# Kernel optimization log

Hardware: AMD Instinct MI355X
Metric: run time of the kernel (lower is better)

Reference implementation:

```python
import jax, jax.numpy as jnp
import numpy as np

# dims
B, L, H, NH, D = 512, 200, 128, 4, 32      # batch, seq_len, hidden, heads (gnn & fcb), head dim H/NH
FT, TP, IP = 32, 64, 200                    # first_taxonomy_num, taxonomy/item nodes per graph
NHOP, NB = 2, 2                             # n_hop gnn layers, gip_block_nums
SH, FH = 512, 256                           # scb_hidden_units, fcb_hidden_units
ITEMS, TAX = 100001, 2000                   # item vocab (+pad row 0), taxonomy vocab
NT, NI = B * TP, B * IP                     # total taxonomy / item nodes in batched forest
DEG_I, DEG_T = 4, 2                         # in-degree per taxonomy node for i2t / t2t edges


def _ln(x, g, b, eps=1e-8):
    m = jnp.mean(x, -1, keepdims=True)
    v = jnp.mean((x - m) ** 2, -1, keepdims=True)
    return (x - m) / jnp.sqrt(v + eps) * g + b


def _gat(src_h, dst_h, es, ed, W, al, ar, bias):
    """DGL GATConv (eval mode): shared fc, leaky_relu(0.2) scores, segment softmax,
    identity residual (in == heads*out), bias, ReLU activation."""
    fs = (src_h @ W).reshape(-1, NH, D)                 # [Ns,NH,D]
    fd = (dst_h @ W).reshape(-1, NH, D)                 # [Nd,NH,D]
    el = jnp.sum(fs * al, -1)                           # [Ns,NH]
    er = jnp.sum(fd * ar, -1)                           # [Nd,NH]
    e = jax.nn.leaky_relu(el[es] + er[ed], 0.2)         # [E,NH]
    emax = jax.ops.segment_max(e, ed, num_segments=NT)
    a = jnp.exp(e - emax[ed])
    s = jax.ops.segment_sum(a, ed, num_segments=NT)
    alpha = a / s[ed]                                   # [E,NH]
    rst = jax.ops.segment_sum(alpha[..., None] * fs[es], ed, num_segments=NT)
    rst = rst + dst_h.reshape(-1, NH, D) + bias.reshape(NH, D)
    return jax.nn.relu(rst).reshape(-1, NH * D)


def _forward(item_embed, tax_embed, scb_ln_g, scb_ln_b, scb_w1, scb_w2, fcb_ln_g, fcb_ln_b,
             fcb_w1, fcb_w2, fcb_w3, wv, gi_w, gi_al, gi_ar, gi_b, gt_w, gt_al, gt_ar, gt_b,
             liw_g, liw_b, int_g, int_b, uni_w,
             seq, root, i2t_src, i2t_dst, t2t_src, t2t_dst, item_ids, tax_ids):
    # --- global intention: mixer-style blocks over the item sequence ---
    V = item_embed[seq]                                           # [B,L,H]
    for i in range(NB):
        nv = _ln(V, scb_ln_g[i], scb_ln_b[i])
        t = jax.nn.gelu(jnp.einsum('blh,ls->bhs', nv, scb_w1[i]), approximate=False)
        vs = nv + jnp.einsum('bhs,sl->blh', t, scb_w2[i])         # seq-mixing block
        nvs = _ln(vs, fcb_ln_g[i], fcb_ln_b[i])
        xh = nvs.reshape(B, L, NH, D)                             # fcb heads share w1/w2
        y = jax.nn.gelu(jnp.einsum('blkc,cf->blkf', xh, fcb_w1[i]), approximate=False)
        y = jnp.einsum('blkf,fc->blkc', y, fcb_w2[i]).reshape(B, L, H)
        V = nvs + y @ fcb_w3[i]
    alpha = jax.nn.softmax(V @ wv, axis=1)                        # [B,L]
    g = jnp.sum(alpha[..., None] * V, axis=1)                     # [B,H]
    # --- local intention: multi-hop hetero GAT on batched item-taxonomy forest ---
    item_h = item_embed[item_ids]                                 # [NI,H]
    tax_h = tax_embed[tax_ids]                                    # [NT,H]
    acc = jnp.zeros_like(tax_h)
    for hop in range(NHOP):
        t_i = _gat(item_h, tax_h, i2t_src, i2t_dst, gi_w[hop], gi_al[hop], gi_ar[hop], gi_b[hop])
        t_t = _gat(tax_h, tax_h, t2t_src, t2t_dst, gt_w[hop], gt_al[hop], gt_ar[hop], gt_b[hop])
        tax_h = t_i + t_t                                         # HeteroGraphConv 'sum'
        acc = acc + tax_h                                         # k_list accumulation
    total = acc / NHOP                                            # average over hops
    offs = jnp.arange(B) * TP                                     # batched-graph offsets (graph_taxonomy)
    valid = root != -1
    local = jnp.where(valid[..., None], total[jnp.clip(root, 0) + offs[:, None]], 0.0)  # [B,FT,H]
    # --- fuse global + local ---
    mul = jnp.einsum('bfh,bh->bf', local, g)                      # [B,FT]
    w = jax.nn.softmax(jnp.where(mul != 0, _ln(mul, liw_g, liw_b), -jnp.inf), axis=-1)
    intention = _ln(g + jnp.sum(w[..., None] * local, axis=1), int_g, int_b)
    return (intention @ uni_w) @ item_embed.T                     # [B, ITEMS]


def setup_inputs():
    key = jax.random.key(0)
    ks = jax.random.split(key, 32)
    nrm = lambda i, sh: jax.random.normal(ks[i], sh, jnp.float32) * 0.05
    inp = {}
    inp['seq'] = jax.random.randint(ks[0], (B, L), 0, ITEMS)
    inp['root'] = jax.random.randint(ks[1], (B, FT), 0, TP)       # all valid roots
    i2t_dst = jnp.repeat(jnp.arange(NT), DEG_I)
    inp['i2t_dst'] = i2t_dst
    inp['i2t_src'] = (i2t_dst // TP) * IP + jax.random.randint(ks[2], (NT * DEG_I,), 0, IP)
    t2t_dst = jnp.repeat(jnp.arange(NT), DEG_T)
    inp['t2t_dst'] = t2t_dst
    inp['t2t_src'] = (t2t_dst // TP) * TP + jax.random.randint(ks[3], (NT * DEG_T,), 0, TP)
    inp['item_ids'] = jax.random.randint(ks[4], (NI,), 1, ITEMS)
    inp['tax_ids'] = jax.random.randint(ks[5], (NT,), 1, TAX)
    inp['item_embed'] = nrm(6, (ITEMS, H)).at[0].set(0.0)         # padding_idx=0
    inp['tax_embed'] = nrm(7, (TAX, H)).at[0].set(0.0)
    inp['scb_ln_g'] = jnp.ones((NB, H)); inp['scb_ln_b'] = jnp.zeros((NB, H))
    inp['scb_w1'] = nrm(8, (NB, L, SH)); inp['scb_w2'] = nrm(9, (NB, SH, L))
    inp['fcb_ln_g'] = jnp.ones((NB, H)); inp['fcb_ln_b'] = jnp.zeros((NB, H))
    inp['fcb_w1'] = nrm(10, (NB, D, FH)); inp['fcb_w2'] = nrm(11, (NB, FH, D))
    inp['fcb_w3'] = nrm(12, (NB, H, H))
    inp['wv'] = nrm(13, (H,))
    inp['gi_w'] = nrm(14, (NHOP, H, H)); inp['gi_al'] = nrm(15, (NHOP, NH, D))
    inp['gi_ar'] = nrm(16, (NHOP, NH, D)); inp['gi_b'] = nrm(17, (NHOP, H))
    inp['gt_w'] = nrm(18, (NHOP, H, H)); inp['gt_al'] = nrm(19, (NHOP, NH, D))
    inp['gt_ar'] = nrm(20, (NHOP, NH, D)); inp['gt_b'] = nrm(21, (NHOP, H))
    inp['liw_g'] = jnp.ones((FT,)); inp['liw_b'] = jnp.zeros((FT,))
    inp['int_g'] = jnp.ones((H,)); inp['int_b'] = jnp.zeros((H,))
    inp['uni_w'] = nrm(22, (H, H))
    return inp


def reference(item_embed, tax_embed, scb_ln_g, scb_ln_b, scb_w1, scb_w2, fcb_ln_g, fcb_ln_b,
              fcb_w1, fcb_w2, fcb_w3, wv, gi_w, gi_al, gi_ar, gi_b, gt_w, gt_al, gt_ar, gt_b,
              liw_g, liw_b, int_g, int_b, uni_w,
              seq, root, i2t_src, i2t_dst, t2t_src, t2t_dst, item_ids, tax_ids):
    return _forward(item_embed, tax_embed, scb_ln_g, scb_ln_b, scb_w1, scb_w2, fcb_ln_g, fcb_ln_b,
                    fcb_w1, fcb_w2, fcb_w3, wv, gi_w, gi_al, gi_ar, gi_b, gt_w, gt_al, gt_ar, gt_b,
                    liw_g, liw_b, int_g, int_b, uni_w,
                    seq, root, i2t_src, i2t_dst, t2t_src, t2t_dst, item_ids, tax_ids)
```

## Files before the change

### kernel.cpp

```cpp
#include <hip/hip_runtime.h>
#include <hip/hip_bf16.h>

constexpr int TB = 512, TL = 200, TH = 128, TNH = 4, TD = 32;
constexpr int TFT = 32, TTP = 64, TIP = 200;
constexpr int TSH = 512, TFH = 256;
constexpr int TITEMS = 100001;
constexpr int TNT = TB * TTP;
constexpr int TNI = TB * TIP;
constexpr int TLP = 224;
constexpr int TIPAD = 100096;

typedef __attribute__((ext_vector_type(8))) short short8v;
typedef __attribute__((ext_vector_type(4))) float f32x4;

__device__ inline float gelu_fast(float x) {
    float u = x + 0.044715f * x * x * x;
    float e = exp2f(-2.302208f * u);
    return x / (1.0f + e);
}
__device__ inline unsigned short to_bf16u(float x) {
    __hip_bfloat16 h = __float2bfloat16(x);
    return *reinterpret_cast<unsigned short*>(&h);
}
__device__ inline float bfu_to_f(unsigned short u) {
    unsigned int x = ((unsigned int)u) << 16;
    return __uint_as_float(x);
}

__device__ inline float block_reduce_sum(float v, float* red) {
    for (int o = 32; o > 0; o >>= 1) v += __shfl_down(v, o, 64);
    int nw = blockDim.x >> 6;
    if ((threadIdx.x & 63) == 0) red[threadIdx.x >> 6] = v;
    __syncthreads();
    float r = 0.f;
    for (int w = 0; w < nw; ++w) r += red[w];
    __syncthreads();
    return r;
}

__global__ __launch_bounds__(256) void k_gather_bf(const float* __restrict__ tab,
                                                   const int* __restrict__ idx,
                                                   unsigned short* __restrict__ out, int nrows) {
    int e = blockIdx.x * blockDim.x + threadIdx.x;
    if (e >= nrows * 16) return;
    int r = e >> 4, c = e & 15;
    const float4 a = ((const float4*)tab)[(size_t)idx[r] * 32 + c * 2];
    const float4 b = ((const float4*)tab)[(size_t)idx[r] * 32 + c * 2 + 1];
    uint4 u;
    u.x = (unsigned int)to_bf16u(a.x) | ((unsigned int)to_bf16u(a.y) << 16);
    u.y = (unsigned int)to_bf16u(a.z) | ((unsigned int)to_bf16u(a.w) << 16);
    u.z = (unsigned int)to_bf16u(b.x) | ((unsigned int)to_bf16u(b.y) << 16);
    u.w = (unsigned int)to_bf16u(b.z) | ((unsigned int)to_bf16u(b.w) << 16);
    *(uint4*)(out + (size_t)e * 8) = u;
}

__global__ __launch_bounds__(256) void k_wcvt(const float* __restrict__ fw1, const float* __restrict__ fw2,
                                              const float* __restrict__ fw3, const float* __restrict__ giw,
                                              const float* __restrict__ gtw, unsigned short* __restrict__ WB) {
    int idx = blockIdx.x * 256 + threadIdx.x;
    float v;
    if (idx < 16384) {
        int nb = idx >> 13, r = idx & 8191, n = r >> 5, k = r & 31;
        v = fw1[(size_t)nb * 8192 + k * 256 + n];
    } else if (idx < 32768) {
        int t = idx - 16384;
        int nb = t >> 13, r = t & 8191, n = r >> 8, k = r & 255;
        v = fw2[(size_t)nb * 8192 + k * 32 + n];
    } else if (idx < 65536) {
        int t = idx - 32768;
        int nb = t >> 14, r = t & 16383, n = r >> 7, k = r & 127;
        v = fw3[(size_t)nb * 16384 + k * 128 + n];
    } else if (idx < 98304) {
        int t = idx - 65536;
        int hop = t >> 14, r = t & 16383, n = r >> 7, k = r & 127;
        v = giw[(size_t)hop * 16384 + k * 128 + n];
    } else {
        int t = idx - 98304;
        int hop = t >> 14, r = t & 16383, n = r >> 7, k = r & 127;
        v = gtw[(size_t)hop * 16384 + k * 128 + n];
    }
    WB[idx] = to_bf16u(v);
}

__global__ __launch_bounds__(128) void k_lnt(const float* __restrict__ V,
                                             const int* __restrict__ seqp, const float* __restrict__ tab,
                                             const float* __restrict__ g, const float* __restrict__ b,
                                             float* __restrict__ NV, unsigned short* __restrict__ NVT) {
    __shared__ float tl[64][129];
    __shared__ float mrow[64], irow[64];
    int bb = blockIdx.y, l0 = blockIdx.x * 64, tid = threadIdx.x;
    for (int i = tid; i < 2048; i += 128) {
        int r = i >> 5, c = i & 31;
        int l = l0 + r;
        float4 v = {0.f, 0.f, 0.f, 0.f};
        if (l < TL) {
            const float* src = seqp ? (tab + (size_t)seqp[bb * TL + l] * TH)
                                    : (V + ((size_t)bb * TL + l) * TH);
            v = *(const float4*)(src + c * 4);
        }
        tl[r][c * 4 + 0] = v.x; tl[r][c * 4 + 1] = v.y;
        tl[r][c * 4 + 2] = v.z; tl[r][c * 4 + 3] = v.w;
    }
    __syncthreads();
    {
        int row = tid >> 1, half = tid & 1;
        float s = 0.f, sq = 0.f;
        for (int k = 0; k < 64; ++k) {
            float v = tl[row][half * 64 + k];
            s += v; sq += v * v;
        }
        s += __shfl_xor(s, 1);
        sq += __shfl_xor(sq, 1);
        if (half == 0) {
            float mean = s * (1.f / 128.f);
            mrow[row] = mean;
            irow[row] = rsqrtf(sq * (1.f / 128.f) - mean * mean + 1e-8f);
        }
    }
    __syncthreads();
    for (int i = tid; i < 2048; i += 128) {
        int r = i >> 5, c = i & 31;
        int l = l0 + r;
        float4 o = {0.f, 0.f, 0.f, 0.f};
        if (l < TL) {
            float4 v = *(float4*)&tl[r][c * 4];
            float m = mrow[r], inv = irow[r];
            const float4 gg = ((const float4*)g)[c];
            const float4 bv = ((const float4*)b)[c];
            o.x = (v.x - m) * inv * gg.x + bv.x;
            o.y = (v.y - m) * inv * gg.y + bv.y;
            o.z = (v.z - m) * inv * gg.z + bv.z;
            o.w = (v.w - m) * inv * gg.w + bv.w;
            *(float4*)(NV + ((size_t)bb * TL + l) * TH + c * 4) = o;
        }
        *(float4*)&tl[r][c * 4] = o;
    }
    __syncthreads();
    int h = tid;
    int ng = (l0 + 64 > TLP) ? (TLP - l0) / 8 : 8;
    for (int lg = 0; lg < ng; ++lg) {
        uint4 u;
        unsigned int p[4];
#pragma unroll
        for (int q = 0; q < 4; ++q) {
            unsigned short ua = to_bf16u(tl[lg * 8 + q * 2 + 0][h]);
            unsigned short ub = to_bf16u(tl[lg * 8 + q * 2 + 1][h]);
            p[q] = (unsigned int)ua | ((unsigned int)ub << 16);
        }
        u.x = p[0]; u.y = p[1]; u.z = p[2]; u.w = p[3];
        *(uint4*)(NVT + ((size_t)bb * TH + h) * TLP + l0 + lg * 8) = u;
    }
}

__global__ __launch_bounds__(256) void k_wscb(const float* __restrict__ w1, const float* __restrict__ w2,
                                              unsigned short* __restrict__ W1T,
                                              unsigned short* __restrict__ W2T) {
    int bx = blockIdx.x;
    if (bx < TSH) {
        int s = bx, l = threadIdx.x;
        if (l < TLP) W1T[(size_t)s * TLP + l] = to_bf16u(l < TL ? w1[(size_t)l * TSH + s] : 0.f);
    } else {
        int l = bx - TSH;
        for (int it = 0; it < 2; ++it) {
            int s = it * 256 + threadIdx.x;
            W2T[(size_t)l * TSH + s] = to_bf16u(l < TL ? w2[(size_t)s * TL + l] : 0.f);
        }
    }
}

__global__ __launch_bounds__(256) void k_mm1(const unsigned short* __restrict__ NVT,
                                             const unsigned short* __restrict__ W1T,
                                             unsigned short* __restrict__ T, int bh) {
    __shared__ unsigned short As[128][40];
    __shared__ unsigned short Bs[128][40];
    int tid = threadIdx.x;
    int b_local = blockIdx.y, b = bh * 256 + b_local;
    int s0 = blockIdx.x * 128;
    int lane = tid & 63, wid = tid >> 6;
    int mw = wid >> 1, nw = wid & 1;
    f32x4 accT[4][4];
#pragma unroll
    for (int j = 0; j < 4; ++j)
#pragma unroll
        for (int i = 0; i < 4; ++i) accT[j][i] = (f32x4){0.f, 0.f, 0.f, 0.f};
    const unsigned short* Abase = NVT + (size_t)b * TH * TLP;
    const unsigned short* Bbase = W1T + (size_t)s0 * TLP;
    for (int kc = 0; kc < 7; ++kc) {
        __syncthreads();
        for (int i = tid; i < 512; i += 256) {
            int r = i >> 2, q = i & 3;
            *(uint4*)&As[r][q * 8] = *(const uint4*)(Abase + (size_t)r * TLP + kc * 32 + q * 8);
            *(uint4*)&Bs[r][q * 8] = *(const uint4*)(Bbase + (size_t)r * TLP + kc * 32 + q * 8);
        }
        __syncthreads();
        int ko = (lane >> 4) * 8;
        short8v af[4], bfr[4];
#pragma unroll
        for (int t = 0; t < 4; ++t) {
            af[t] = *(const short8v*)&As[mw * 64 + t * 16 + (lane & 15)][ko];
            bfr[t] = *(const short8v*)&Bs[nw * 64 + t * 16 + (lane & 15)][ko];
        }
#pragma unroll
        for (int j = 0; j < 4; ++j)
#pragma unroll
            for (int i = 0; i < 4; ++i)
                accT[j][i] = __builtin_amdgcn_mfma_f32_16x16x32_bf16(bfr[j], af[i], accT[j][i], 0, 0, 0);
    }
    int rbase = (lane >> 4) * 4, col = lane & 15;
#pragma unroll
    for (int i = 0; i < 4; ++i)
#pragma unroll
        for (int j = 0; j < 4; ++j) {
            int h = mw * 64 + i * 16 + col;
            int sb = s0 + nw * 64 + j * 16 + rbase;
            ushort4 pk;
            pk.x = to_bf16u(gelu_fast(accT[j][i][0]));
            pk.y = to_bf16u(gelu_fast(accT[j][i][1]));
            pk.z = to_bf16u(gelu_fast(accT[j][i][2]));
            pk.w = to_bf16u(gelu_fast(accT[j][i][3]));
            *(ushort4*)(T + ((size_t)b_local * TH + h) * TSH + sb) = pk;
        }
}

__global__ __launch_bounds__(256) void k_mm2l(const unsigned short* __restrict__ T,
                                              const unsigned short* __restrict__ W2T,
                                              float* __restrict__ NV,
                                              const float* __restrict__ lg, const float* __restrict__ lb,
                                              int bh) {
    __shared__ unsigned short As[128][40];
    __shared__ unsigned short Bs[64][40];
    __shared__ float vsl[64][132];
    __shared__ float mrow[64], irow[64];
    int tid = threadIdx.x;
    int b_local = blockIdx.y, b = bh * 256 + b_local;
    int l0 = blockIdx.x * 64;
    int lane = tid & 63, wid = tid >> 6;
    f32x4 acc[2][4];
#pragma unroll
    for (int i = 0; i < 2; ++i)
#pragma unroll
        for (int j = 0; j < 4; ++j) acc[i][j] = (f32x4){0.f, 0.f, 0.f, 0.f};
    const unsigned short* Abase = T + (size_t)b_local * TH * TSH;
    for (int kc = 0; kc < 16; ++kc) {
        __syncthreads();
        for (int i = tid; i < 512; i += 256) {
            int r = i >> 2, q = i & 3;
            *(uint4*)&As[r][q * 8] = *(const uint4*)(Abase + (size_t)r * TSH + kc * 32 + q * 8);
        }
        {
            int r = tid >> 2, q = tid & 3;
            int l = l0 + r;
            uint4 v = {0u, 0u, 0u, 0u};
            if (l < 208) v = *(const uint4*)(W2T + (size_t)l * TSH + kc * 32 + q * 8);
            *(uint4*)&Bs[r][q * 8] = v;
        }
        __syncthreads();
        int ko = (lane >> 4) * 8;
        short8v af[2], bfr[4];
#pragma unroll
        for (int t = 0; t < 2; ++t)
            af[t] = *(const short8v*)&As[wid * 32 + t * 16 + (lane & 15)][ko];
#pragma unroll
        for (int j = 0; j < 4; ++j)
            bfr[j] = *(const short8v*)&Bs[j * 16 + (lane & 15)][ko];
#pragma unroll
        for (int i = 0; i < 2; ++i)
#pragma unroll
            for (int j = 0; j < 4; ++j)
                acc[i][j] = __builtin_amdgcn_mfma_f32_16x16x32_bf16(af[i], bfr[j], acc[i][j], 0, 0, 0);
    }
    int rbase = (lane >> 4) * 4, col = lane & 15;
#pragma unroll
    for (int i = 0; i < 2; ++i)
#pragma unroll
        for (int j = 0; j < 4; ++j) {
            int l = l0 + j * 16 + col;
            int h0 = wid * 32 + i * 16 + rbase;
            float4 res = {0.f, 0.f, 0.f, 0.f};
            if (l < TL) res = *(const float4*)(NV + ((size_t)b * TL + l) * TH + h0);
            float4 o;
            o.x = acc[i][j][0] + res.x;
            o.y = acc[i][j][1] + res.y;
            o.z = acc[i][j][2] + res.z;
            o.w = acc[i][j][3] + res.w;
            *(float4*)&vsl[j * 16 + col][h0] = o;
        }
    __syncthreads();
    int row = tid >> 2, q = tid & 3;
    {
        float s = 0.f, sq = 0.f;
        for (int k = 0; k < 32; ++k) {
            float v = vsl[row][q * 32 + k];
            s += v; sq += v * v;
        }
        s += __shfl_xor(s, 1); s += __shfl_xor(s, 2);
        sq += __shfl_xor(sq, 1); sq += __shfl_xor(sq, 2);
        if (q == 0) {
            float mean = s * (1.f / 128.f);
            mrow[row] = mean;
            irow[row] = rsqrtf(sq * (1.f / 128.f) - mean * mean + 1e-8f);
        }
    }
    __syncthreads();
    {
        int l = l0 + row;
        if (l < TL) {
            float mean = mrow[row], inv = irow[row];
            float* dst = NV + ((size_t)b * TL + l) * TH + q * 32;
#pragma unroll
            for (int k4 = 0; k4 < 8; ++k4) {
                float4 v = *(float4*)&vsl[row][q * 32 + k4 * 4];
                const float4 gg = ((const float4*)lg)[q * 8 + k4];
                const float4 bv = ((const float4*)lb)[q * 8 + k4];
                float4 o;
                o.x = (v.x - mean) * inv * gg.x + bv.x;
                o.y = (v.y - mean) * inv * gg.y + bv.y;
                o.z = (v.z - mean) * inv * gg.z + bv.z;
                o.w = (v.w - mean) * inv * gg.w + bv.w;
                *(float4*)(dst + k4 * 4) = o;
            }
        }
    }
}

__global__ __launch_bounds__(256) void k_ffuse(const float* __restrict__ NV,
                                               const unsigned short* __restrict__ FW1B,
                                               const unsigned short* __restrict__ FW2B,
                                               unsigned short* __restrict__ Z) {
    __shared__ unsigned short As[64][40];
    __shared__ unsigned short BsBuf[256 * 40];
    __shared__ unsigned short Yl[64 * 264];
    int tid = threadIdx.x;
    int m0 = blockIdx.x * 64;
    int lane = tid & 63, wid = tid >> 6;
    int col = lane & 15, rbase = (lane >> 4) * 4, ko = (lane >> 4) * 8;
    for (int i = tid; i < 512; i += 256) {
        int r = i >> 3, q = i & 7;
        const float4 v = *(const float4*)(NV + (size_t)(m0 + r) * 32 + q * 4);
        ushort4 u;
        u.x = to_bf16u(v.x); u.y = to_bf16u(v.y); u.z = to_bf16u(v.z); u.w = to_bf16u(v.w);
        *(ushort4*)&As[r][q * 4] = u;
    }
    for (int i = tid; i < 1024; i += 256) {
        int r = i >> 2, q = i & 3;
        *(uint4*)&BsBuf[r * 40 + q * 8] = *(const uint4*)(FW1B + r * 32 + q * 8);
    }
    __syncthreads();
    short8v af[4], bfr[4];
#pragma unroll
    for (int t = 0; t < 4; ++t) {
        af[t] = *(const short8v*)&As[t * 16 + col][ko];
        bfr[t] = *(const short8v*)&BsBuf[(wid * 64 + t * 16 + col) * 40 + ko];
    }
    __syncthreads();
    {
        f32x4 yt[4][4];
#pragma unroll
        for (int j = 0; j < 4; ++j)
#pragma unroll
            for (int i = 0; i < 4; ++i) yt[j][i] = (f32x4){0.f, 0.f, 0.f, 0.f};
#pragma unroll
        for (int j = 0; j < 4; ++j)
#pragma unroll
            for (int i = 0; i < 4; ++i)
                yt[j][i] = __builtin_amdgcn_mfma_f32_16x16x32_bf16(bfr[j], af[i], yt[j][i], 0, 0, 0);
#pragma unroll
        for (int i = 0; i < 4; ++i)
#pragma unroll
            for (int j = 0; j < 4; ++j) {
                int m = i * 16 + col;
                int n0 = wid * 64 + j * 16 + rbase;
                ushort4 pk;
                pk.x = to_bf16u(gelu_fast(yt[j][i][0]));
                pk.y = to_bf16u(gelu_fast(yt[j][i][1]));
                pk.z = to_bf16u(gelu_fast(yt[j][i][2]));
                pk.w = to_bf16u(gelu_fast(yt[j][i][3]));
                int idx = (m * 264 + n0) ^ (((m >> 2) & 7) << 3);
                *(ushort4*)&Yl[idx] = pk;
            }
    }
    for (int i = tid; i < 1024; i += 256) {
        int r = i >> 5, q = i & 31;
        *(uint4*)&BsBuf[r * 264 + q * 8] = *(const uint4*)(FW2B + r * 256 + q * 8);
    }
    __syncthreads();
    {
        f32x4 acc2[2];
        acc2[0] = (f32x4){0.f, 0.f, 0.f, 0.f};
        acc2[1] = (f32x4){0.f, 0.f, 0.f, 0.f};
        int mrow = wid * 16 + col;
        int sw = ((mrow >> 2) & 7) << 3;
        for (int kc = 0; kc < 8; ++kc) {
            int ko2 = kc * 32 + ko;
            short8v a2 = *(const short8v*)&Yl[(mrow * 264 + ko2) ^ sw];
            short8v b0 = *(const short8v*)&BsBuf[col * 264 + ko2];
            short8v b1 = *(const short8v*)&BsBuf[(16 + col) * 264 + ko2];
            acc2[0] = __builtin_amdgcn_mfma_f32_16x16x32_bf16(a2, b0, acc2[0], 0, 0, 0);
            acc2[1] = __builtin_amdgcn_mfma_f32_16x16x32_bf16(a2, b1, acc2[1], 0, 0, 0);
        }
#pragma unroll
        for (int j = 0; j < 2; ++j)
#pragma unroll
            for (int r = 0; r < 4; ++r)
                Z[(size_t)(m0 + wid * 16 + rbase + r) * 32 + j * 16 + col] =
                    to_bf16u(acc2[j][r]);
    }
}

__global__ __launch_bounds__(256) void k_gmm_b(const unsigned short* __restrict__ A,
                                               const unsigned short* __restrict__ WB,
                                               const float* __restrict__ R,
                                               float* __restrict__ C) {
    __shared__ unsigned short As[128][40];
    __shared__ unsigned short Bs[128][40];
    int tid = threadIdx.x;
    int m0 = blockIdx.x * 128;
    int lane = tid & 63, wid = tid >> 6;
    int mw = wid >> 1, nw = wid & 1;
    f32x4 acc[4][4];
#pragma unroll
    for (int i = 0; i < 4; ++i)
#pragma unroll
        for (int j = 0; j < 4; ++j) acc[i][j] = (f32x4){0.f, 0.f, 0.f, 0.f};
    for (int kc = 0; kc < 4; ++kc) {
        __syncthreads();
        for (int i = tid; i < 512; i += 256) {
            int r = i >> 2, q = i & 3;
            *(uint4*)&As[r][q * 8] = *(const uint4*)(A + (size_t)(m0 + r) * TH + kc * 32 + q * 8);
            *(uint4*)&Bs[r][q * 8] = *(const uint4*)(WB + (size_t)r * TH + kc * 32 + q * 8);
        }
        __syncthreads();
        int ko = (lane >> 4) * 8;
        short8v af[4], bfr[4];
#pragma unroll
        for (int t = 0; t < 4; ++t) {
            af[t] = *(const short8v*)&As[mw * 64 + t * 16 + (lane & 15)][ko];
            bfr[t] = *(const short8v*)&Bs[nw * 64 + t * 16 + (lane & 15)][ko];
        }
#pragma unroll
        for (int i = 0; i < 4; ++i)
#pragma unroll
            for (int j = 0; j < 4; ++j)
                acc[i][j] = __builtin_amdgcn_mfma_f32_16x16x32_bf16(af[i], bfr[j], acc[i][j], 0, 0, 0);
    }
    int rbase = (lane >> 4) * 4, col = lane & 15;
#pragma unroll
    for (int i = 0; i < 4; ++i)
#pragma unroll
        for (int j = 0; j < 4; ++j) {
            int n = nw * 64 + j * 16 + col;
#pragma unroll
            for (int r = 0; r < 4; ++r) {
                size_t off = (size_t)(m0 + mw * 64 + i * 16 + rbase + r) * TH + n;
                float v = acc[i][j][r];
                if (R) v += R[off];
                C[off] = v;
            }
        }
}

__global__ __launch_bounds__(256) void k_gmm_bb(const unsigned short* __restrict__ A,
                                                const unsigned short* __restrict__ WB,
                                                unsigned short* __restrict__ C) {
    __shared__ unsigned short As[128][40];
    __shared__ unsigned short Bs[128][40];
    int tid = threadIdx.x;
    int m0 = blockIdx.x * 128;
    int lane = tid & 63, wid = tid >> 6;
    int mw = wid >> 1, nw = wid & 1;
    f32x4 accT[4][4];
#pragma unroll
    for (int j = 0; j < 4; ++j)
#pragma unroll
        for (int i = 0; i < 4; ++i) accT[j][i] = (f32x4){0.f, 0.f, 0.f, 0.f};
    for (int kc = 0; kc < 4; ++kc) {
        __syncthreads();
        for (int i = tid; i < 512; i += 256) {
            int r = i >> 2, q = i & 3;
            *(uint4*)&As[r][q * 8] = *(const uint4*)(A + (size_t)(m0 + r) * TH + kc * 32 + q * 8);
            *(uint4*)&Bs[r][q * 8] = *(const uint4*)(WB + (size_t)r * TH + kc * 32 + q * 8);
        }
        __syncthreads();
        int ko = (lane >> 4) * 8;
        short8v af[4], bfr[4];
#pragma unroll
        for (int t = 0; t < 4; ++t) {
            af[t] = *(const short8v*)&As[mw * 64 + t * 16 + (lane & 15)][ko];
            bfr[t] = *(const short8v*)&Bs[nw * 64 + t * 16 + (lane & 15)][ko];
        }
#pragma unroll
        for (int j = 0; j < 4; ++j)
#pragma unroll
            for (int i = 0; i < 4; ++i)
                accT[j][i] = __builtin_amdgcn_mfma_f32_16x16x32_bf16(bfr[j], af[i], accT[j][i], 0, 0, 0);
    }
    int rbase = (lane >> 4) * 4, col = lane & 15;
#pragma unroll
    for (int i = 0; i < 4; ++i)
#pragma unroll
        for (int j = 0; j < 4; ++j) {
            int m = m0 + mw * 64 + i * 16 + col;
            int n0 = nw * 64 + j * 16 + rbase;
            ushort4 pk;
            pk.x = to_bf16u(accT[j][i][0]);
            pk.y = to_bf16u(accT[j][i][1]);
            pk.z = to_bf16u(accT[j][i][2]);
            pk.w = to_bf16u(accT[j][i][3]);
            *(ushort4*)(C + (size_t)m * TH + n0) = pk;
        }
}

__global__ __launch_bounds__(256) void k_pool(const float* __restrict__ V, const float* __restrict__ wv,
                                              float* __restrict__ g) {
    __shared__ float sc[TL];
    __shared__ float red[4];
    int b = blockIdx.x, tid = threadIdx.x;
    int lane = tid & 63, w = tid >> 6;
    for (int l = w; l < TL; l += 4) {
        const float2 v = ((const float2*)(V + (size_t)(b * TL + l) * TH))[lane];
        float a = v.x * wv[2 * lane] + v.y * wv[2 * lane + 1];
        for (int o = 32; o > 0; o >>= 1) a += __shfl_down(a, o, 64);
        if (lane == 0) sc[l] = a;
    }
    __syncthreads();
    float m = (tid < TL) ? sc[tid] : -INFINITY;
    for (int o = 32; o > 0; o >>= 1) m = fmaxf(m, __shfl_down(m, o, 64));
    if ((tid & 63) == 0) red[tid >> 6] = m;
    __syncthreads();
    m = fmaxf(fmaxf(red[0], red[1]), fmaxf(red[2], red[3]));
    __syncthreads();
    float e = (tid < TL) ? expf(sc[tid] - m) : 0.f;
    float s = block_reduce_sum(e, red);
    if (tid < TL) sc[tid] = e / s;
    __syncthreads();
    if (tid < TH) {
        float a = 0.f;
        for (int l = 0; l < TL; ++l) a += sc[l] * V[(size_t)(b * TL + l) * TH + tid];
        g[b * TH + tid] = a;
    }
}

__global__ __launch_bounds__(256) void k_scores4(
        const unsigned short* __restrict__ f0, const float* __restrict__ v0, float* __restrict__ o0, int n0,
        const unsigned short* __restrict__ f1, const float* __restrict__ v1, float* __restrict__ o1, int n1,
        const unsigned short* __restrict__ f2, const float* __restrict__ v2, float* __restrict__ o2, int n2,
        const unsigned short* __restrict__ f3, const float* __restrict__ v3, float* __restrict__ o3, int n3) {
    int t = blockIdx.x * 256 + threadIdx.x;
    const unsigned short* f; const float* vec; float* o;
    if (t < n0 * 4) { f = f0; vec = v0; o = o0; }
    else {
        t -= n0 * 4;
        if (t < n1 * 4) { f = f1; vec = v1; o = o1; }
        else {
            t -= n1 * 4;
            if (t < n2 * 4) { f = f2; vec = v2; o = o2; }
            else {
                t -= n2 * 4;
                if (t >= n3 * 4) return;
                f = f3; vec = v3; o = o3;
            }
        }
    }
    int node = t >> 2, k = t & 3;
    const unsigned short* fp = f + (size_t)node * TH + k * TD;
    const float* vp = vec + k * TD;
    float a = 0.f;
#pragma unroll
    for (int q = 0; q < 4; ++q) {
        uint4 u = *(const uint4*)(fp + q * 8);
        unsigned int ws[4] = {u.x, u.y, u.z, u.w};
#pragma unroll
        for (int p = 0; p < 4; ++p) {
            a += __uint_as_float(ws[p] << 16) * vp[q * 8 + p * 2];
            a += __uint_as_float(ws[p] & 0xffff0000u) * vp[q * 8 + p * 2 + 1];
        }
    }
    o[t] = a;
}

__global__ __launch_bounds__(128) void k_gat(const unsigned short* __restrict__ tax_cur,
                                             const unsigned short* __restrict__ fs_i, const float* __restrict__ el_i,
                                             const float* __restrict__ er_i, const int* __restrict__ src_i,
                                             const float* __restrict__ bi,
                                             const unsigned short* __restrict__ fs_t, const float* __restrict__ el_t,
                                             const float* __restrict__ er_t, const int* __restrict__ src_t,
                                             const float* __restrict__ bt,
                                             unsigned short* __restrict__ tax_nxt,
                                             float* __restrict__ acc, int hop) {
    int n = blockIdx.x, h = threadIdx.x, k = h >> 5;
    float cur = bfu_to_f(tax_cur[(size_t)n * TH + h]);
    float ti, tt2;
    {
        float er = er_i[n * 4 + k];
        int s[4]; float e[4]; float m = -INFINITY;
#pragma unroll
        for (int j = 0; j < 4; ++j) {
            s[j] = src_i[n * 4 + j];
            float xx = el_i[s[j] * 4 + k] + er;
            e[j] = xx > 0.f ? xx : 0.2f * xx;
            m = fmaxf(m, e[j]);
        }
        float ssum = 0.f, av = 0.f;
#pragma unroll
        for (int j = 0; j < 4; ++j) {
            float a = expf(e[j] - m);
            ssum += a;
            av += a * bfu_to_f(fs_i[(size_t)s[j] * TH + h]);
        }
        ti = fmaxf(av / ssum + cur + bi[h], 0.f);
    }
    {
        float er = er_t[n * 4 + k];
        int s[2]; float e[2]; float m = -INFINITY;
#pragma unroll
        for (int j = 0; j < 2; ++j) {
            s[j] = src_t[n * 2 + j];
            float xx = el_t[s[j] * 4 + k] + er;
            e[j] = xx > 0.f ? xx : 0.2f * xx;
            m = fmaxf(m, e[j]);
        }
        float ssum = 0.f, av = 0.f;
#pragma unroll
        for (int j = 0; j < 2; ++j) {
            float a = expf(e[j] - m);
            ssum += a;
            av += a * bfu_to_f(fs_t[(size_t)s[j] * TH + h]);
        }
        tt2 = fmaxf(av / ssum + cur + bt[h], 0.f);
    }
    float nx = ti + tt2;
    size_t ai = (size_t)n * TH + h;
    tax_nxt[ai] = to_bf16u(nx);
    acc[ai] = (hop == 0) ? nx : acc[ai] + nx;
}

__global__ __launch_bounds__(128) void k_locfuse(const int* __restrict__ root, const float* __restrict__ acc,
                                                 const float* __restrict__ g,
                                                 const float* __restrict__ liw_g, const float* __restrict__ liw_b,
                                                 const float* __restrict__ int_g, const float* __restrict__ int_b,
                                                 const float* __restrict__ uni_w,
                                                 unsigned short* __restrict__ PB) {
    __shared__ float loc[TFT][TH];
    __shared__ float lm[TFT], wv_[TFT], inten[TH];
    __shared__ float red[2];
    int b = blockIdx.x, tid = threadIdx.x;
    float gv = g[b * TH + tid];
    for (int f = 0; f < TFT; ++f) {
        int r = root[b * TFT + f];
        float v = 0.f;
        if (r != -1) v = acc[(size_t)(b * TTP + (r < 0 ? 0 : r)) * TH + tid] * 0.5f;
        loc[f][tid] = v;
        float s = block_reduce_sum(v * gv, red);
        if (tid == 0) lm[f] = s;
    }
    __syncthreads();
    if (tid < TFT) {
        float mean = 0.f;
        for (int f = 0; f < TFT; ++f) mean += lm[f];
        mean *= (1.f / TFT);
        float var = 0.f;
        for (int f = 0; f < TFT; ++f) { float d = lm[f] - mean; var += d * d; }
        var *= (1.f / TFT);
        float ln = (lm[tid] - mean) * rsqrtf(var + 1e-8f) * liw_g[tid] + liw_b[tid];
        wv_[tid] = (lm[tid] != 0.f) ? ln : -INFINITY;
    }
    __syncthreads();
    if (tid < TFT) {
        float mx = -INFINITY;
        for (int f = 0; f < TFT; ++f) mx = fmaxf(mx, wv_[f]);
        float s = 0.f;
        for (int f = 0; f < TFT; ++f) s += expf(wv_[f] - mx);
        lm[tid] = expf(wv_[tid] - mx) / s;
    }
    __syncthreads();
    float ip = gv;
    for (int f = 0; f < TFT; ++f) ip += lm[f] * loc[f][tid];
    float mean = block_reduce_sum(ip, red) * (1.f / TH);
    float d = ip - mean;
    float var = block_reduce_sum(d * d, red) * (1.f / TH);
    inten[tid] = d * rsqrtf(var + 1e-8f) * int_g[tid] + int_b[tid];
    __syncthreads();
    float a = 0.f;
    for (int hp = 0; hp < TH; ++hp) a += inten[hp] * uni_w[hp * TH + tid];
    PB[(size_t)b * TH + tid] = to_bf16u(a);
}

__global__ __launch_bounds__(256) void k_ebc(const float* __restrict__ E,
                                             unsigned short* __restrict__ EB) {
    int t = blockIdx.x * 256 + threadIdx.x;
    if (t >= TIPAD * TH / 8) return;
    size_t base = (size_t)t * 8;
    int row = (int)(base >> 7);
    float4 a = {0.f, 0.f, 0.f, 0.f}, b = {0.f, 0.f, 0.f, 0.f};
    if (row < TITEMS) {
        a = *(const float4*)(E + base);
        b = *(const float4*)(E + base + 4);
    }
    ushort4 u0, u1;
    u0.x = to_bf16u(a.x); u0.y = to_bf16u(a.y); u0.z = to_bf16u(a.z); u0.w = to_bf16u(a.w);
    u1.x = to_bf16u(b.x); u1.y = to_bf16u(b.y); u1.z = to_bf16u(b.z); u1.w = to_bf16u(b.w);
    *(ushort4*)(EB + base) = u0;
    *(ushort4*)(EB + base + 4) = u1;
}

__global__ __launch_bounds__(256) void k_final_m(const unsigned short* __restrict__ PB,
                                                 const unsigned short* __restrict__ EB,
                                                 float* __restrict__ out) {
    __shared__ unsigned short Bs[128][136];
    int tid = threadIdx.x;
    int i0 = blockIdx.x * 128, b0 = blockIdx.y * 128;
    for (int i = tid; i < 2048; i += 256) {
        int r = i >> 4, q = i & 15;
        *(uint4*)&Bs[r][q * 8] = *(const uint4*)(EB + (size_t)(i0 + r) * TH + q * 8);
    }
    __syncthreads();
    int lane = tid & 63, wid = tid >> 6;
    int mw = wid >> 1, nw = wid & 1;
    f32x4 acc[4][4];
#pragma unroll
    for (int i = 0; i < 4; ++i)
#pragma unroll
        for (int j = 0; j < 4; ++j) acc[i][j] = (f32x4){0.f, 0.f, 0.f, 0.f};
#pragma unroll
    for (int kc = 0; kc < 4; ++kc) {
        int ko = kc * 32 + (lane >> 4) * 8;
        short8v af[4], bfr[4];
#pragma unroll
        for (int t = 0; t < 4; ++t) {
            af[t] = *(const short8v*)(PB + (size_t)(b0 + mw * 64 + t * 16 + (lane & 15)) * TH + ko);
            bfr[t] = *(const short8v*)&Bs[nw * 64 + t * 16 + (lane & 15)][ko];
        }
#pragma unroll
        for (int i = 0; i < 4; ++i)
#pragma unroll
            for (int j = 0; j < 4; ++j)
                acc[i][j] = __builtin_amdgcn_mfma_f32_16x16x32_bf16(af[i], bfr[j], acc[i][j], 0, 0, 0);
    }
    int rbase = (lane >> 4) * 4, col = lane & 15;
#pragma unroll
    for (int i = 0; i < 4; ++i)
#pragma unroll
        for (int j = 0; j < 4; ++j) {
            int ii = i0 + nw * 64 + j * 16 + col;
            if (ii < TITEMS) {
#pragma unroll
                for (int r = 0; r < 4; ++r)
                    out[(size_t)(b0 + mw * 64 + i * 16 + rbase + r) * TITEMS + ii] = acc[i][j][r];
            }
        }
}

extern "C" void kernel_launch(void* const* d_in, const int* in_sizes, int n_in,
                              void* d_out, int out_size, void* d_ws, size_t ws_size,
                              hipStream_t stream) {
    const int*   seq        = (const int*)d_in[0];
    const int*   root       = (const int*)d_in[1];
    const int*   i2t_src    = (const int*)d_in[3];
    const int*   t2t_src    = (const int*)d_in[5];
    const int*   item_ids   = (const int*)d_in[6];
    const int*   tax_ids    = (const int*)d_in[7];
    const float* item_embed = (const float*)d_in[8];
    const float* tax_embed  = (const float*)d_in[9];
    const float* scb_ln_g   = (const float*)d_in[10];
    const float* scb_ln_b   = (const float*)d_in[11];
    const float* scb_w1     = (const float*)d_in[12];
    const float* scb_w2     = (const float*)d_in[13];
    const float* fcb_ln_g   = (const float*)d_in[14];
    const float* fcb_ln_b   = (const float*)d_in[15];
    const float* fcb_w1     = (const float*)d_in[16];
    const float* fcb_w2     = (const float*)d_in[17];
    const float* fcb_w3     = (const float*)d_in[18];
    const float* wv         = (const float*)d_in[19];
    const float* gi_w       = (const float*)d_in[20];
    const float* gi_al      = (const float*)d_in[21];
    const float* gi_ar      = (const float*)d_in[22];
    const float* gi_b       = (const float*)d_in[23];
    const float* gt_w       = (const float*)d_in[24];
    const float* gt_al      = (const float*)d_in[25];
    const float* gt_ar      = (const float*)d_in[26];
    const float* gt_b       = (const float*)d_in[27];
    const float* liw_g      = (const float*)d_in[28];
    const float* liw_b      = (const float*)d_in[29];
    const float* int_g      = (const float*)d_in[30];
    const float* int_b      = (const float*)d_in[31];
    const float* uni_w      = (const float*)d_in[32];

    char* w = (char*)d_ws;
    float* V     = (float*)(w + 0);
    float* NV    = (float*)(w + 52428800);
    unsigned short* FSIB   = (unsigned short*)(w + 0);
    unsigned short* ITEMHB = (unsigned short*)(w + 52428800);
    unsigned short* NVT = (unsigned short*)(w + 104857600);
    unsigned short* T   = (unsigned short*)(w + 134217728);
    unsigned short* W1T = (unsigned short*)(w + 167772160);
    unsigned short* W2T = (unsigned short*)(w + 168001536);
    unsigned short* ZB  = (unsigned short*)(w + 104857600);
    unsigned short* TAXB0 = (unsigned short*)(w + 104857600);
    unsigned short* TAXB1 = (unsigned short*)(w + 113246208);
    float* ACC   = (float*)(w + 138412032);
    unsigned short* FDIB = (unsigned short*)(w + 155189248);
    unsigned short* FSTB = (unsigned short*)(w + 171966464);
    float* ELI   = (float*)(w + 188743680);
    float* ERI   = (float*)(w + 190382080);
    float* ELT   = (float*)(w + 190906368);
    float* ERT   = (float*)(w + 191430656);
    float* G     = (float*)(w + 200343552);
    unsigned short* WB = (unsigned short*)(w + 191954944);
    unsigned short* EB = (unsigned short*)(w + 155189248);
    unsigned short* PB = (unsigned short*)(w + 200671232);
    if (ws_size < 200933376ull) return;

    k_wcvt<<<512, 256, 0, stream>>>(fcb_w1, fcb_w2, fcb_w3, gi_w, gt_w, WB);

    for (int nb = 0; nb < 2; ++nb) {
        k_lnt<<<dim3(4, TB), 128, 0, stream>>>(V, nb == 0 ? seq : nullptr, item_embed,
                                               scb_ln_g + nb * TH, scb_ln_b + nb * TH, NV, NVT);
        k_wscb<<<720, 256, 0, stream>>>(scb_w1 + nb * TL * TSH, scb_w2 + nb * TSH * TL, W1T, W2T);
        for (int bh = 0; bh < 2; ++bh) {
            k_mm1<<<dim3(4, 256), 256, 0, stream>>>(NVT, W1T, T, bh);
            k_mm2l<<<dim3(4, 256), 256, 0, stream>>>(T, W2T, NV,
                                                     fcb_ln_g + nb * TH, fcb_ln_b + nb * TH, bh);
        }
        k_ffuse<<<TB * TL * 4 / 64, 256, 0, stream>>>(NV, WB + nb * 8192, WB + 16384 + nb * 8192, ZB);
        k_gmm_b<<<TB * TL / 128, 256, 0, stream>>>(ZB, WB + 32768 + nb * 16384, NV, V);
    }
    k_pool<<<TB, 256, 0, stream>>>(V, wv, G);

    k_gather_bf<<<(TNI * 16 + 255) / 256, 256, 0, stream>>>(item_embed, item_ids, ITEMHB, TNI);
    k_gather_bf<<<(TNT * 16 + 255) / 256, 256, 0, stream>>>(tax_embed, tax_ids, TAXB0, TNT);

    unsigned short* curb = TAXB0;
    unsigned short* nxtb = TAXB1;
    for (int hop = 0; hop < 2; ++hop) {
        const unsigned short* WiB = WB + 65536 + hop * 16384;
        const unsigned short* WtB = WB + 98304 + hop * 16384;
        k_gmm_bb<<<TNI / 128, 256, 0, stream>>>(ITEMHB, WiB, FSIB);
        k_gmm_bb<<<TNT / 128, 256, 0, stream>>>(curb, WiB, FDIB);
        k_gmm_bb<<<TNT / 128, 256, 0, stream>>>(curb, WtB, FSTB);
        int total = (TNI + 3 * TNT) * TNH;
        k_scores4<<<(total + 255) / 256, 256, 0, stream>>>(
            FSIB, gi_al + hop * TH, ELI, TNI,
            FDIB, gi_ar + hop * TH, ERI, TNT,
            FSTB, gt_al + hop * TH, ELT, TNT,
            FSTB, gt_ar + hop * TH, ERT, TNT);
        k_gat<<<TNT, 128, 0, stream>>>(curb, FSIB, ELI, ERI, i2t_src, gi_b + hop * TH,
                                       FSTB, ELT, ERT, t2t_src, gt_b + hop * TH, nxtb, ACC, hop);
        unsigned short* tmp = curb; curb = nxtb; nxtb = tmp;
    }

    k_locfuse<<<TB, 128, 0, stream>>>(root, ACC, G, liw_g, liw_b, int_g, int_b, uni_w, PB);
    k_ebc<<<(TIPAD * TH / 8 + 255) / 256, 256, 0, stream>>>(item_embed, EB);
    k_final_m<<<dim3(TIPAD / 128, TB / 128), 256, 0, stream>>>(PB, EB, (float*)d_out);
}
```

Baseline: 1.028 ms.

## Persist ffuse weights, batch GAT GEMMs, fuse embedding cast into final matmul

k_ffuse becomes a persistent kernel: it loads both weight tiles into shared memory once, then loops over row tiles, so weights are no longer reloaded per tile. The three per-hop GEMMs are merged into one launch that picks its operands from the block index. The separate bf16 conversion of the item embedding table is removed; the final matmul converts fp32 embeddings to bf16 inside each block and loops over all batch tiles, so each embedding tile is read once. These changes cut launch overhead and a full write and read of the converted table, at the cost of fewer blocks in the final kernel (782) and serial work across the four batch tiles.

```diff
diff --git a/kernel.cpp b/kernel.cpp
--- a/kernel.cpp
+++ b/kernel.cpp
@@ -326,84 +326,90 @@
 __global__ __launch_bounds__(256) void k_ffuse(const float* __restrict__ NV,
                                                const unsigned short* __restrict__ FW1B,
                                                const unsigned short* __restrict__ FW2B,
-                                               unsigned short* __restrict__ Z) {
+                                               unsigned short* __restrict__ Z, int ntiles) {
     __shared__ unsigned short As[64][40];
-    __shared__ unsigned short BsBuf[256 * 40];
+    __shared__ unsigned short Bs2[32 * 264];
     __shared__ unsigned short Yl[64 * 264];
     int tid = threadIdx.x;
-    int m0 = blockIdx.x * 64;
     int lane = tid & 63, wid = tid >> 6;
     int col = lane & 15, rbase = (lane >> 4) * 4, ko = (lane >> 4) * 8;
-    for (int i = tid; i < 512; i += 256) {
-        int r = i >> 3, q = i & 7;
-        const float4 v = *(const float4*)(NV + (size_t)(m0 + r) * 32 + q * 4);
-        ushort4 u;
-        u.x = to_bf16u(v.x); u.y = to_bf16u(v.y); u.z = to_bf16u(v.z); u.w = to_bf16u(v.w);
-        *(ushort4*)&As[r][q * 4] = u;
-    }
     for (int i = tid; i < 1024; i += 256) {
         int r = i >> 2, q = i & 3;
-        *(uint4*)&BsBuf[r * 40 + q * 8] = *(const uint4*)(FW1B + r * 32 + q * 8);
-    }
-    __syncthreads();
-    short8v af[4], bfr[4];
-#pragma unroll
-    for (int t = 0; t < 4; ++t) {
-        af[t] = *(const short8v*)&As[t * 16 + col][ko];
-        bfr[t] = *(const short8v*)&BsBuf[(wid * 64 + t * 16 + col) * 40 + ko];
-    }
-    __syncthreads();
-    {
-        f32x4 yt[4][4];
-#pragma unroll
-        for (int j = 0; j < 4; ++j)
-#pragma unroll
-            for (int i = 0; i < 4; ++i) yt[j][i] = (f32x4){0.f, 0.f, 0.f, 0.f};
-#pragma unroll
-        for (int j = 0; j < 4; ++j)
-#pragma unroll
-            for (int i = 0; i < 4; ++i)
-                yt[j][i] = __builtin_amdgcn_mfma_f32_16x16x32_bf16(bfr[j], af[i], yt[j][i], 0, 0, 0);
-#pragma unroll
-        for (int i = 0; i < 4; ++i)
-#pragma unroll
-            for (int j = 0; j < 4; ++j) {
-                int m = i * 16 + col;
-                int n0 = wid * 64 + j * 16 + rbase;
-                ushort4 pk;
-                pk.x = to_bf16u(gelu_fast(yt[j][i][0]));
-                pk.y = to_bf16u(gelu_fast(yt[j][i][1]));
-                pk.z = to_bf16u(gelu_fast(yt[j][i][2]));
-                pk.w = to_bf16u(gelu_fast(yt[j][i][3]));
-                int idx = (m * 264 + n0) ^ (((m >> 2) & 7) << 3);
-                *(ushort4*)&Yl[idx] = pk;
-            }
+        *(uint4*)&Yl[r * 40 + q * 8] = *(const uint4*)(FW1B + r * 32 + q * 8);
     }
     for (int i = tid; i < 1024; i += 256) {
         int r = i >> 5, q = i & 31;
-        *(uint4*)&BsBuf[r * 264 + q * 8] = *(const uint4*)(FW2B + r * 256 + q * 8);
-    }
-    __syncthreads();
-    {
-        f32x4 acc2[2];
-        acc2[0] = (f32x4){0.f, 0.f, 0.f, 0.f};
-        acc2[1] = (f32x4){0.f, 0.f, 0.f, 0.f};
-        int mrow = wid * 16 + col;
-        int sw = ((mrow >> 2) & 7) << 3;
-        for (int kc = 0; kc < 8; ++kc) {
-            int ko2 = kc * 32 + ko;
-            short8v a2 = *(const short8v*)&Yl[(mrow * 264 + ko2) ^ sw];
-            short8v b0 = *(const short8v*)&BsBuf[col * 264 + ko2];
-            short8v b1 = *(const short8v*)&BsBuf[(16 + col) * 264 + ko2];
-            acc2[0] = __builtin_amdgcn_mfma_f32_16x16x32_bf16(a2, b0, acc2[0], 0, 0, 0);
-            acc2[1] = __builtin_amdgcn_mfma_f32_16x16x32_bf16(a2, b1, acc2[1], 0, 0, 0);
-        }
-#pragma unroll
-        for (int j = 0; j < 2; ++j)
-#pragma unroll
-            for (int r = 0; r < 4; ++r)
-                Z[(size_t)(m0 + wid * 16 + rbase + r) * 32 + j * 16 + col] =
-                    to_bf16u(acc2[j][r]);
+        *(uint4*)&Bs2[r * 264 + q * 8] = *(const uint4*)(FW2B + r * 256 + q * 8);
+    }
+    __syncthreads();
+    short8v bfr[4];
+#pragma unroll
+    for (int t = 0; t < 4; ++t)
+        bfr[t] = *(const short8v*)&Yl[(wid * 64 + t * 16 + col) * 40 + ko];
+    __syncthreads();
+    int mrow = wid * 16 + col;
+    int sw2 = ((mrow >> 2) & 7) << 3;
+    for (int tile = blockIdx.x; tile < ntiles; tile += gridDim.x) {
+        int m0 = tile * 64;
+        for (int i = tid; i < 512; i += 256) {
+            int r = i >> 3, q = i & 7;
+            const float4 v = *(const float4*)(NV + (size_t)(m0 + r) * 32 + q * 4);
+            ushort4 u;
+            u.x = to_bf16u(v.x); u.y = to_bf16u(v.y); u.z = to_bf16u(v.z); u.w = to_bf16u(v.w);
+            *(ushort4*)&As[r][q * 4] = u;
+        }
+        __syncthreads();
+        {
+            short8v af[4];
+#pragma unroll
+            for (int t = 0; t < 4; ++t)
+                af[t] = *(const short8v*)&As[t * 16 + col][ko];
+            f32x4 yt[4][4];
+#pragma unroll
+            for (int j = 0; j < 4; ++j)
+#pragma unroll
+                for (int i = 0; i < 4; ++i) yt[j][i] = (f32x4){0.f, 0.f, 0.f, 0.f};
+#pragma unroll
+            for (int j = 0; j < 4; ++j)
+#pragma unroll
+                for (int i = 0; i < 4; ++i)
+                    yt[j][i] = __builtin_amdgcn_mfma_f32_16x16x32_bf16(bfr[j], af[i], yt[j][i], 0, 0, 0);
+#pragma unroll
+            for (int i = 0; i < 4; ++i)
+#pragma unroll
+                for (int j = 0; j < 4; ++j) {
+                    int m = i * 16 + col;
+                    int n0 = wid * 64 + j * 16 + rbase;
+                    ushort4 pk;
+                    pk.x = to_bf16u(gelu_fast(yt[j][i][0]));
+                    pk.y = to_bf16u(gelu_fast(yt[j][i][1]));
+                    pk.z = to_bf16u(gelu_fast(yt[j][i][2]));
+                    pk.w = to_bf16u(gelu_fast(yt[j][i][3]));
+                    int idx = (m * 264 + n0) ^ (((m >> 2) & 7) << 3);
+                    *(ushort4*)&Yl[idx] = pk;
+                }
+        }
+        __syncthreads();
+        {
+            f32x4 acc2[2];
+            acc2[0] = (f32x4){0.f, 0.f, 0.f, 0.f};
+            acc2[1] = (f32x4){0.f, 0.f, 0.f, 0.f};
+            for (int kc = 0; kc < 8; ++kc) {
+                int ko2 = kc * 32 + ko;
+                short8v a2 = *(const short8v*)&Yl[(mrow * 264 + ko2) ^ sw2];
+                short8v b0 = *(const short8v*)&Bs2[col * 264 + ko2];
+                short8v b1 = *(const short8v*)&Bs2[(16 + col) * 264 + ko2];
+                acc2[0] = __builtin_amdgcn_mfma_f32_16x16x32_bf16(a2, b0, acc2[0], 0, 0, 0);
+                acc2[1] = __builtin_amdgcn_mfma_f32_16x16x32_bf16(a2, b1, acc2[1], 0, 0, 0);
+            }
+#pragma unroll
+            for (int j = 0; j < 2; ++j)
+#pragma unroll
+                for (int r = 0; r < 4; ++r)
+                    Z[(size_t)(m0 + wid * 16 + rbase + r) * 32 + j * 16 + col] =
+                        to_bf16u(acc2[j][r]);
+        }
+        __syncthreads();
     }
 }
 
@@ -459,13 +465,23 @@
         }
 }
 
-__global__ __launch_bounds__(256) void k_gmm_bb(const unsigned short* __restrict__ A,
-                                                const unsigned short* __restrict__ WB,
-                                                unsigned short* __restrict__ C) {
+__global__ __launch_bounds__(256) void k_gmm3(
+        const unsigned short* __restrict__ A0, const unsigned short* __restrict__ W0,
+        unsigned short* __restrict__ C0, int nb0,
+        const unsigned short* __restrict__ A1, const unsigned short* __restrict__ W1,
+        unsigned short* __restrict__ C1, int nb1,
+        const unsigned short* __restrict__ A2, const unsigned short* __restrict__ W2,
+        unsigned short* __restrict__ C2) {
     __shared__ unsigned short As[128][40];
     __shared__ unsigned short Bs[128][40];
+    int bx = blockIdx.x;
+    const unsigned short *A, *WBp;
+    unsigned short* C;
+    if (bx < nb0) { A = A0; WBp = W0; C = C0; }
+    else if (bx - nb0 < nb1) { bx -= nb0; A = A1; WBp = W1; C = C1; }
+    else { bx -= nb0 + nb1; A = A2; WBp = W2; C = C2; }
     int tid = threadIdx.x;
-    int m0 = blockIdx.x * 128;
+    int m0 = bx * 128;
     int lane = tid & 63, wid = tid >> 6;
     int mw = wid >> 1, nw = wid & 1;
     f32x4 accT[4][4];
@@ -478,7 +494,7 @@
         for (int i = tid; i < 512; i += 256) {
             int r = i >> 2, q = i & 3;
             *(uint4*)&As[r][q * 8] = *(const uint4*)(A + (size_t)(m0 + r) * TH + kc * 32 + q * 8);
-            *(uint4*)&Bs[r][q * 8] = *(const uint4*)(WB + (size_t)r * TH + kc * 32 + q * 8);
+            *(uint4*)&Bs[r][q * 8] = *(const uint4*)(WBp + (size_t)r * TH + kc * 32 + q * 8);
         }
         __syncthreads();
         int ko = (lane >> 4) * 8;
@@ -685,69 +701,64 @@
     PB[(size_t)b * TH + tid] = to_bf16u(a);
 }
 
-__global__ __launch_bounds__(256) void k_ebc(const float* __restrict__ E,
-                                             unsigned short* __restrict__ EB) {
-    int t = blockIdx.x * 256 + threadIdx.x;
-    if (t >= TIPAD * TH / 8) return;
-    size_t base = (size_t)t * 8;
-    int row = (int)(base >> 7);
-    float4 a = {0.f, 0.f, 0.f, 0.f}, b = {0.f, 0.f, 0.f, 0.f};
-    if (row < TITEMS) {
-        a = *(const float4*)(E + base);
-        b = *(const float4*)(E + base + 4);
-    }
-    ushort4 u0, u1;
-    u0.x = to_bf16u(a.x); u0.y = to_bf16u(a.y); u0.z = to_bf16u(a.z); u0.w = to_bf16u(a.w);
-    u1.x = to_bf16u(b.x); u1.y = to_bf16u(b.y); u1.z = to_bf16u(b.z); u1.w = to_bf16u(b.w);
-    *(ushort4*)(EB + base) = u0;
-    *(ushort4*)(EB + base + 4) = u1;
-}
-
-__global__ __launch_bounds__(256) void k_final_m(const unsigned short* __restrict__ PB,
-                                                 const unsigned short* __restrict__ EB,
-                                                 float* __restrict__ out) {
+__global__ __launch_bounds__(256) void k_final_m2(const unsigned short* __restrict__ PB,
+                                                  const float* __restrict__ E,
+                                                  float* __restrict__ out) {
     __shared__ unsigned short Bs[128][136];
     int tid = threadIdx.x;
-    int i0 = blockIdx.x * 128, b0 = blockIdx.y * 128;
+    int i0 = blockIdx.x * 128;
     for (int i = tid; i < 2048; i += 256) {
         int r = i >> 4, q = i & 15;
-        *(uint4*)&Bs[r][q * 8] = *(const uint4*)(EB + (size_t)(i0 + r) * TH + q * 8);
+        int it = i0 + r;
+        float4 a = {0.f, 0.f, 0.f, 0.f}, b = {0.f, 0.f, 0.f, 0.f};
+        if (it < TITEMS) {
+            a = *(const float4*)(E + (size_t)it * TH + q * 8);
+            b = *(const float4*)(E + (size_t)it * TH + q * 8 + 4);
+        }
+        ushort4 u0, u1;
+        u0.x = to_bf16u(a.x); u0.y = to_bf16u(a.y); u0.z = to_bf16u(a.z); u0.w = to_bf16u(a.w);
+        u1.x = to_bf16u(b.x); u1.y = to_bf16u(b.y); u1.z = to_bf16u(b.z); u1.w = to_bf16u(b.w);
+        *(ushort4*)&Bs[r][q * 8] = u0;
+        *(ushort4*)&Bs[r][q * 8 + 4] = u1;
     }
     __syncthreads();
     int lane = tid & 63, wid = tid >> 6;
     int mw = wid >> 1, nw = wid & 1;
-    f32x4 acc[4][4];
-#pragma unroll
-    for (int i = 0; i < 4; ++i)
-#pragma unroll
-        for (int j = 0; j < 4; ++j) acc[i][j] = (f32x4){0.f, 0.f, 0.f, 0.f};
-#pragma unroll
-    for (int kc = 0; kc < 4; ++kc) {
-        int ko = kc * 32 + (lane >> 4) * 8;
-        short8v af[4], bfr[4];
-#pragma unroll
-        for (int t = 0; t < 4; ++t) {
-            af[t] = *(const short8v*)(PB + (size_t)(b0 + mw * 64 + t * 16 + (lane & 15)) * TH + ko);
-            bfr[t] = *(const short8v*)&Bs[nw * 64 + t * 16 + (lane & 15)][ko];
-        }
+    int rbase = (lane >> 4) * 4, col = lane & 15;
+#pragma unroll 1
+    for (int b0 = 0; b0 < TB; b0 += 128) {
+        f32x4 acc[4][4];
 #pragma unroll
         for (int i = 0; i < 4; ++i)
 #pragma unroll
-            for (int j = 0; j < 4; ++j)
-                acc[i][j] = __builtin_amdgcn_mfma_f32_16x16x32_bf16(af[i], bfr[j], acc[i][j], 0, 0, 0);
-    }
-    int rbase = (lane >> 4) * 4, col = lane & 15;
-#pragma unroll
-    for (int i = 0; i < 4; ++i)
-#pragma unroll
-        for (int j = 0; j < 4; ++j) {
-            int ii = i0 + nw * 64 + j * 16 + col;
-            if (ii < TITEMS) {
-#pragma unroll
-                for (int r = 0; r < 4; ++r)
-                    out[(size_t)(b0 + mw * 64 + i * 16 + rbase + r) * TITEMS + ii] = acc[i][j][r];
+            for (int j = 0; j < 4; ++j) acc[i][j] = (f32x4){0.f, 0.f, 0.f, 0.f};
+#pragma unroll
+        for (int kc = 0; kc < 4; ++kc) {
+            int ko = kc * 32 + (lane >> 4) * 8;
+            short8v af[4], bfr[4];
+#pragma unroll
+            for (int t = 0; t < 4; ++t) {
+                af[t] = *(const short8v*)(PB + (size_t)(b0 + mw * 64 + t * 16 + (lane & 15)) * TH + ko);
+                bfr[t] = *(const short8v*)&Bs[nw * 64 + t * 16 + (lane & 15)][ko];
             }
-        }
+#pragma unroll
+            for (int i = 0; i < 4; ++i)
+#pragma unroll
+                for (int j = 0; j < 4; ++j)
+                    acc[i][j] = __builtin_amdgcn_mfma_f32_16x16x32_bf16(af[i], bfr[j], acc[i][j], 0, 0, 0);
+        }
+#pragma unroll
+        for (int i = 0; i < 4; ++i)
+#pragma unroll
+            for (int j = 0; j < 4; ++j) {
+                int ii = i0 + nw * 64 + j * 16 + col;
+                if (ii < TITEMS) {
+#pragma unroll
+                    for (int r = 0; r < 4; ++r)
+                        out[(size_t)(b0 + mw * 64 + i * 16 + rbase + r) * TITEMS + ii] = acc[i][j][r];
+                }
+            }
+    }
 }
 
 extern "C" void kernel_launch(void* const* d_in, const int* in_sizes, int n_in,
@@ -806,7 +817,6 @@
     float* ERT   = (float*)(w + 191430656);
     float* G     = (float*)(w + 200343552);
     unsigned short* WB = (unsigned short*)(w + 191954944);
-    unsigned short* EB = (unsigned short*)(w + 155189248);
     unsigned short* PB = (unsigned short*)(w + 200671232);
     if (ws_size < 200933376ull) return;
 
@@ -821,7 +831,8 @@
             k_mm2l<<<dim3(4, 256), 256, 0, stream>>>(T, W2T, NV,
                                                      fcb_ln_g + nb * TH, fcb_ln_b + nb * TH, bh);
         }
-        k_ffuse<<<TB * TL * 4 / 64, 256, 0, stream>>>(NV, WB + nb * 8192, WB + 16384 + nb * 8192, ZB);
+        k_ffuse<<<1024, 256, 0, stream>>>(NV, WB + nb * 8192, WB + 16384 + nb * 8192, ZB,
+                                          TB * TL * 4 / 64);
         k_gmm_b<<<TB * TL / 128, 256, 0, stream>>>(ZB, WB + 32768 + nb * 16384, NV, V);
     }
     k_pool<<<TB, 256, 0, stream>>>(V, wv, G);
@@ -834,9 +845,10 @@
     for (int hop = 0; hop < 2; ++hop) {
         const unsigned short* WiB = WB + 65536 + hop * 16384;
         const unsigned short* WtB = WB + 98304 + hop * 16384;
-        k_gmm_bb<<<TNI / 128, 256, 0, stream>>>(ITEMHB, WiB, FSIB);
-        k_gmm_bb<<<TNT / 128, 256, 0, stream>>>(curb, WiB, FDIB);
-        k_gmm_bb<<<TNT / 128, 256, 0, stream>>>(curb, WtB, FSTB);
+        k_gmm3<<<TNI / 128 + 2 * (TNT / 128), 256, 0, stream>>>(
+            ITEMHB, WiB, FSIB, TNI / 128,
+            curb, WiB, FDIB, TNT / 128,
+            curb, WtB, FSTB);
         int total = (TNI + 3 * TNT) * TNH;
         k_scores4<<<(total + 255) / 256, 256, 0, stream>>>(
             FSIB, gi_al + hop * TH, ELI, TNI,
@@ -849,6 +861,5 @@
     }
 
     k_locfuse<<<TB, 128, 0, stream>>>(root, ACC, G, liw_g, liw_b, int_g, int_b, uni_w, PB);
-    k_ebc<<<(TIPAD * TH / 8 + 255) / 256, 256, 0, stream>>>(item_embed, EB);
-    k_final_m<<<dim3(TIPAD / 128, TB / 128), 256, 0, stream>>>(PB, EB, (float*)d_out);
-}
+    k_final_m2<<<TIPAD / 128, 256, 0, stream>>>(PB, item_embed, (float*)d_out);
+}
```

After: 1.002 ms. 2.5% less time.
